# Performance work log

Measured on AMD Instinct MI355X. Metric: run time of the kernel, lower is better.

The kernel has to match this reference:

```python
import jax, jax.numpy as jnp
import numpy as np
import math

LENGTH = 2048
N_LEVEL = int(math.log2(LENGTH))   # 11 butterfly levels
BATCH = 4096
CROSS_T = 1.0      # crossing_transmission_factor (ideal)
CROSS_PHI = 0.0    # crossing_phase_shift (ideal)


def _bitrev(n):
    perm = np.arange(n).reshape(n, 1)
    for _ in range(int(math.log2(n))):
        h = perm.shape[0] // 2
        perm = np.hstack((perm[:h], perm[h:]))
    return perm.squeeze(0)


def _forward_indices(length):
    # ButterflyPermutation.gen_permutation_indices (forward direction)
    nlev = int(math.log2(length)) - 1
    init = np.arange(length)
    idxs = []
    for level in range(nlev):
        bs = 2 ** (level + 2)
        idx = init.reshape(-1, length // bs, 2, bs // 2).transpose(0, 1, 3, 2).reshape(-1)
        idxs.append(idx)
    return idxs


def _crossings(idxs, length):
    # cascaded waveguide-crossing transfer function per level: [length, 2] complex
    out = []
    for idx in idxs:
        n = np.abs(idx - np.arange(length)).astype(np.float32)
        mag = CROSS_T ** n
        phi = n * CROSS_PHI
        out.append(np.stack([mag * np.cos(phi), mag * np.sin(phi)], -1).astype(np.float32))
    return out


BITREV = _bitrev(LENGTH)
FWD_IDX = _forward_indices(LENGTH)
CROSSINGS = [jnp.asarray(c) for c in _crossings(FWD_IDX, LENGTH)]


def complex_mult(a, b):
    ar, ai = a[..., 0], a[..., 1]
    br, bi = b[..., 0], b[..., 1]
    return jnp.stack([ar * br - ai * bi, ar * bi + ai * br], axis=-1)


def setup_inputs() -> dict:
    key = jax.random.key(0)
    kx, kp = jax.random.split(key)
    x = jax.random.normal(kx, (BATCH, LENGTH, 2), dtype=jnp.float32)
    phases = jax.random.normal(kp, (N_LEVEL + 1, LENGTH // 2, 2), dtype=jnp.float32)
    return {"x": x, "phases": phases}


def reference(x, phases):
    # mode='full' coupler transfer function (build_coupler_transfer_function_2)
    ph = phases[:N_LEVEL]                      # [n_level, L/2, 2]
    c1, c2 = jnp.cos(ph[..., 0]), jnp.cos(ph[..., 1])
    s1, s2 = jnp.sin(ph[..., 0]), jnp.sin(ph[..., 1])
    w_real = jnp.stack([c1, -s2, -s1, c2], -1).reshape(N_LEVEL, LENGTH // 2, 2, 2)
    w_imag = jnp.stack([s1, c2, c1, s2], -1).reshape(N_LEVEL, LENGTH // 2, 2, 2)

    out = x[:, BITREV, :]                      # bit-reversal permutation
    for level in range(N_LEVEL):
        v = out.reshape(BATCH, LENGTH // 2, 2, 2)   # [b, pair, j, complex]
        vr, vi = v[..., 0], v[..., 1]
        wr, wi = w_real[level], w_imag[level]
        # complex 2x2 matvec per pair
        r = jnp.einsum('pij,bpj->bpi', wr, vr) - jnp.einsum('pij,bpj->bpi', wi, vi)
        i = jnp.einsum('pij,bpj->bpi', wr, vi) + jnp.einsum('pij,bpj->bpi', wi, vr)
        out = jnp.stack([r, i], -1).reshape(BATCH, LENGTH, 2)
        if level < N_LEVEL - 1:
            # butterfly permutation + crossing transfer (identity when ideal)
            out = complex_mult(CROSSINGS[level][None], out[:, FWD_IDX[level], :])

    # last-level phase shifter: one phase per waveguide
    lp = phases[-1].reshape(LENGTH)
    ps = jnp.stack([jnp.cos(lp), jnp.sin(lp)], -1)  # [L, 2]
    return complex_mult(ps[None], out)
```

## Files before the change

### kernel.cpp

```cpp
#include <hip/hip_runtime.h>


__device__ __forceinline__ unsigned revw(unsigned x, int w) {
    return w ? (__brev(x) >> (32 - w)) : 0u;
}
__device__ __forceinline__ unsigned pmap(unsigned slot, int level) {
    int shift = 10 - level;
    return (revw(slot & ((1u << shift) - 1u), shift) << level) | (slot >> (shift + 1));
}

__global__ void twiddle_kernel(const float* __restrict__ phases, float4* __restrict__ tw) {
    int id = blockIdx.x * 256 + threadIdx.x;
    if (id >= 12288) return;
    float t1, t2;
    if (id < 2048) {
        int t = id & 255, r = id >> 8;
        int b = r & 1, pj = (r >> 1) & 1, lvl = r >> 2;
        unsigned unit = (unsigned)t + ((lvl == 0) ? 256u : 512u) * (unsigned)pj;
        unsigned slot = 2u * unit + (unsigned)b;
        unsigned p = pmap(slot, lvl);
        t1 = phases[(lvl * 1024 + p) * 2 + 0];
        t2 = phases[(lvl * 1024 + p) * 2 + 1];
    } else if (id < 8192) {
        int j2 = id - 2048;
        int sg = j2 / 3072, rem = j2 % 3072;
        int m = rem >> 8, t = rem & 255;
        int L = 2 + 3 * sg;
        int lg = sg ? 3 : 6;
        unsigned H = 1u << lg;
        unsigned s = (((unsigned)t >> lg) << (lg + 3)) | ((unsigned)t & (H - 1));
        int lo = m >> 2, pj = m & 3;
        int j = (lo == 0) ? pj : ((lo == 1) ? ((pj & 1) | ((pj >> 1) << 2)) : (pj << 1));
        unsigned slot = s + (unsigned)j * H;
        int level = L + lo;
        unsigned p = pmap(slot, level);
        t1 = phases[(level * 1024 + p) * 2 + 0];
        t2 = phases[(level * 1024 + p) * 2 + 1];
    } else if (id < 9216) {
        unsigned u = (unsigned)(id - 8192);
        unsigned c0 = 2u * u, c1 = 2u * u + 1u;
        t1 = phases[(8 * 1024 + pmap(c0 & ~4u, 8)) * 2 + ((c0 >> 2) & 1)];
        t2 = phases[(8 * 1024 + pmap(c1 & ~4u, 8)) * 2 + ((c1 >> 2) & 1)];
    } else if (id < 10240) {
        unsigned u = (unsigned)(id - 9216);
        unsigned c0 = 2u * u, c1 = 2u * u + 1u;
        t1 = phases[(9 * 1024 + pmap(c0 & ~2u, 9)) * 2 + ((c0 >> 1) & 1)];
        t2 = phases[(9 * 1024 + pmap(c1 & ~2u, 9)) * 2 + ((c1 >> 1) & 1)];
    } else if (id < 11264) {
        unsigned u = (unsigned)(id - 10240);
        unsigned p = pmap(2u * u, 10);
        t1 = phases[(10 * 1024 + p) * 2 + 0];
        t2 = phases[(10 * 1024 + p) * 2 + 1];
    } else {
        int q = id - 11264;
        t1 = phases[11 * 2048 + q * 2 + 0];
        t2 = phases[11 * 2048 + q * 2 + 1];
    }
    tw[id] = make_float4(cosf(t1), sinf(t1), cosf(t2), sinf(t2));
}

__device__ __forceinline__ void bf(float2 v0, float2 v1, float4 w, float2& o0, float2& o1) {
    float ar = fmaf(w.x, v0.x, -w.y * v0.y);
    float ai = fmaf(w.x, v0.y,  w.y * v0.x);
    float br = fmaf(w.z, v1.x, -w.w * v1.y);
    float bi = fmaf(w.z, v1.y,  w.w * v1.x);
    o0 = make_float2(ar - bi, ai + br);
    o1 = make_float2(br - ai, bi + ar);
}
__device__ __forceinline__ float2 cm(float wc, float ws, float2 z) {
    return make_float2(fmaf(wc, z.x, -ws * z.y), fmaf(wc, z.y, ws * z.x));
}
__device__ __forceinline__ float2 comb(float2 local, float2 recv) {
    return make_float2(local.x - recv.y, local.y + recv.x);
}
__device__ __forceinline__ float2 sx(float2 v, int mask) {
    return make_float2(__shfl_xor(v.x, mask, 64), __shfl_xor(v.y, mask, 64));
}

__device__ __forceinline__ void lvlA(float2 e[8], const float4 w[4]) {
    bf(e[0], e[4], w[0], e[0], e[4]);
    bf(e[1], e[5], w[1], e[1], e[5]);
    bf(e[2], e[6], w[2], e[2], e[6]);
    bf(e[3], e[7], w[3], e[3], e[7]);
}
__device__ __forceinline__ void lvlB(float2 e[8], const float4 w[4]) {
    bf(e[0], e[2], w[0], e[0], e[2]);
    bf(e[1], e[3], w[1], e[1], e[3]);
    bf(e[4], e[6], w[2], e[4], e[6]);
    bf(e[5], e[7], w[3], e[5], e[7]);
}
__device__ __forceinline__ void lvlC(float2 e[8], const float4 w[4]) {
    bf(e[0], e[1], w[0], e[0], e[1]);
    bf(e[2], e[3], w[1], e[2], e[3]);
    bf(e[4], e[5], w[2], e[4], e[5]);
    bf(e[6], e[7], w[3], e[6], e[7]);
}

__device__ __forceinline__ void lbar() {
    asm volatile("s_waitcnt lgkmcnt(0)" ::: "memory");
    __builtin_amdgcn_s_barrier();
}

__global__ __launch_bounds__(256, 4) void bfly_kernel(const float4* __restrict__ x,
                                                      const float4* __restrict__ tw,
                                                      float4* __restrict__ out) {
    __shared__ float4 lds[2048];
    float2* lf = (float2*)lds;
    const unsigned t = threadIdx.x;
    const int rowbase = blockIdx.x * 2048;

    float2 z0[8], z1[8];
    float4 w[4], wn[4];

    {
        const float4* x0 = x + rowbase;
        const float4* x1 = x + rowbase + 1024;
#pragma unroll
        for (int k = 0; k < 4; ++k) {
            float4 u = x0[t + 256u * k];
            z0[2 * k] = make_float2(u.x, u.y); z0[2 * k + 1] = make_float2(u.z, u.w);
        }
#pragma unroll
        for (int k = 0; k < 4; ++k) {
            float4 u = x1[t + 256u * k];
            z1[2 * k] = make_float2(u.x, u.y); z1[2 * k + 1] = make_float2(u.z, u.w);
        }
#pragma unroll
        for (int k = 0; k < 4; ++k) w[k] = tw[k * 256 + t];
        lvlA(z0, w); lvlA(z1, w);
#pragma unroll
        for (int k = 0; k < 4; ++k) w[k] = tw[(4 + k) * 256 + t];
        lvlB(z0, w); lvlB(z1, w);
#pragma unroll
        for (int m = 0; m < 4; ++m) wn[m] = tw[2048 + m * 256 + t];
#pragma unroll
        for (int k = 0; k < 4; ++k) {
            lds[t + 256u * k]        = make_float4(z0[2 * k].x, z0[2 * k].y, z0[2 * k + 1].x, z0[2 * k + 1].y);
            lds[1024 + t + 256u * k] = make_float4(z1[2 * k].x, z1[2 * k].y, z1[2 * k + 1].x, z1[2 * k + 1].y);
        }
    }
    lbar();

    {
        const unsigned s = ((t >> 6) << 9) | (t & 63u);
        float4 wb[4], wc[4];
#pragma unroll
        for (int m = 0; m < 4; ++m) wb[m] = tw[2048 + (4 + m) * 256 + t];
#pragma unroll
        for (int m = 0; m < 4; ++m) wc[m] = tw[2048 + (8 + m) * 256 + t];
#pragma unroll
        for (int j = 0; j < 8; ++j) z0[j] = lf[s + 64u * j];
#pragma unroll
        for (int j = 0; j < 8; ++j) z1[j] = lf[2048 + s + 64u * j];
        lvlA(z0, wn); lvlA(z1, wn);
        lvlB(z0, wb); lvlB(z1, wb);
        lvlC(z0, wc); lvlC(z1, wc);
#pragma unroll
        for (int m = 0; m < 4; ++m) wn[m] = tw[5120 + m * 256 + t];
#pragma unroll
        for (int j = 0; j < 8; ++j) lf[s + 64u * j] = z0[j];
#pragma unroll
        for (int j = 0; j < 8; ++j) lf[2048 + s + 64u * j] = z1[j];
    }
    lbar();

    {
        const unsigned s2 = ((t >> 3) << 6) | (t & 7u);
        float4 wb[4], wc[4];
#pragma unroll
        for (int m = 0; m < 4; ++m) wb[m] = tw[5120 + (4 + m) * 256 + t];
#pragma unroll
        for (int m = 0; m < 4; ++m) wc[m] = tw[5120 + (8 + m) * 256 + t];
#pragma unroll
        for (int j = 0; j < 8; ++j) z0[j] = lf[s2 + 8u * j];
#pragma unroll
        for (int j = 0; j < 8; ++j) z1[j] = lf[2048 + s2 + 8u * j];
        lvlA(z0, wn); lvlA(z1, wn);
        lvlB(z0, wb); lvlB(z1, wb);
        lvlC(z0, wc); lvlC(z1, wc);
#pragma unroll
        for (int g = 0; g < 4; ++g) wn[g] = tw[8192 + t + 256u * g];
#pragma unroll
        for (int j = 0; j < 8; ++j) lf[s2 + 8u * j] = z0[j];
#pragma unroll
        for (int j = 0; j < 8; ++j) lf[2048 + s2 + 8u * j] = z1[j];
    }
    lbar();

#pragma unroll
    for (int g = 0; g < 4; ++g) {
        const unsigned u = t + 256u * g;
        float4 w9 = tw[9216 + u];
        float4 wA = tw[10240 + u];
        float4 p  = tw[11264 + u];
        float4 q0 = lds[u];
        float4 q1 = lds[1024 + u];
        float2 x00 = make_float2(q0.x, q0.y), x01 = make_float2(q0.z, q0.w);
        float2 x10 = make_float2(q1.x, q1.y), x11 = make_float2(q1.z, q1.w);
        float4 w8 = wn[g];
        float2 a00 = cm(w8.x, w8.y, x00), a01 = cm(w8.z, w8.w, x01);
        float2 a10 = cm(w8.x, w8.y, x10), a11 = cm(w8.z, w8.w, x11);
        x00 = comb(a00, sx(a00, 2)); x01 = comb(a01, sx(a01, 2));
        x10 = comb(a10, sx(a10, 2)); x11 = comb(a11, sx(a11, 2));
        a00 = cm(w9.x, w9.y, x00); a01 = cm(w9.z, w9.w, x01);
        a10 = cm(w9.x, w9.y, x10); a11 = cm(w9.z, w9.w, x11);
        x00 = comb(a00, sx(a00, 1)); x01 = comb(a01, sx(a01, 1));
        x10 = comb(a10, sx(a10, 1)); x11 = comb(a11, sx(a11, 1));
        bf(x00, x01, wA, x00, x01);
        bf(x10, x11, wA, x10, x11);
        out[rowbase + u] = make_float4(
            fmaf(p.x, x00.x, -p.y * x00.y), fmaf(p.x, x00.y, p.y * x00.x),
            fmaf(p.z, x01.x, -p.w * x01.y), fmaf(p.z, x01.y, p.w * x01.x));
        out[rowbase + 1024 + u] = make_float4(
            fmaf(p.x, x10.x, -p.y * x10.y), fmaf(p.x, x10.y, p.y * x10.x),
            fmaf(p.z, x11.x, -p.w * x11.y), fmaf(p.z, x11.y, p.w * x11.x));
    }
}

extern "C" void kernel_launch(void* const* d_in, const int* in_sizes, int n_in,
                              void* d_out, int out_size, void* d_ws, size_t ws_size,
                              hipStream_t stream) {
    const float* x = (const float*)d_in[0];
    const float* phases = (const float*)d_in[1];
    float4* tw = (float4*)d_ws;

    twiddle_kernel<<<48, 256, 0, stream>>>(phases, tw);
    bfly_kernel<<<2048, 256, 0, stream>>>((const float4*)x, tw, (float4*)d_out);
}
```

Measured before the change: 42.41 us.

## Interleave paired rows in LDS as float4 with XOR swizzle

Shared memory is relaid so each float4 slot holds the same complex element from both rows a block processes. The middle stages then issue one 128-bit LDS access per element instead of two 64-bit ones, and an XOR swizzle on the slot index is meant to spread the strided accesses across banks. Launch bounds are also raised from 4 to 5 waves per SIMD. The higher occupancy target tightens the register budget and could cause spills.

```diff
diff --git a/kernel.cpp b/kernel.cpp
--- a/kernel.cpp
+++ b/kernel.cpp
@@ -96,16 +96,17 @@
     bf(e[6], e[7], w[3], e[6], e[7]);
 }
 
+__device__ __forceinline__ unsigned swz(unsigned U) { return U ^ ((U >> 3) & 7u); }
+
 __device__ __forceinline__ void lbar() {
     asm volatile("s_waitcnt lgkmcnt(0)" ::: "memory");
     __builtin_amdgcn_s_barrier();
 }
 
-__global__ __launch_bounds__(256, 4) void bfly_kernel(const float4* __restrict__ x,
+__global__ __launch_bounds__(256, 5) void bfly_kernel(const float4* __restrict__ x,
                                                       const float4* __restrict__ tw,
                                                       float4* __restrict__ out) {
-    __shared__ float4 lds[2048];
-    float2* lf = (float2*)lds;
+    __shared__ float4 lds4[2048];
     const unsigned t = threadIdx.x;
     const int rowbase = blockIdx.x * 2048;
 
@@ -135,8 +136,9 @@
         for (int m = 0; m < 4; ++m) wn[m] = tw[2048 + m * 256 + t];
 #pragma unroll
         for (int k = 0; k < 4; ++k) {
-            lds[t + 256u * k]        = make_float4(z0[2 * k].x, z0[2 * k].y, z0[2 * k + 1].x, z0[2 * k + 1].y);
-            lds[1024 + t + 256u * k] = make_float4(z1[2 * k].x, z1[2 * k].y, z1[2 * k + 1].x, z1[2 * k + 1].y);
+            unsigned c = 2u * (t + 256u * k);
+            lds4[swz(c)]     = make_float4(z0[2 * k].x, z0[2 * k].y, z1[2 * k].x, z1[2 * k].y);
+            lds4[swz(c + 1)] = make_float4(z0[2 * k + 1].x, z0[2 * k + 1].y, z1[2 * k + 1].x, z1[2 * k + 1].y);
         }
     }
     lbar();
@@ -149,18 +151,18 @@
 #pragma unroll
         for (int m = 0; m < 4; ++m) wc[m] = tw[2048 + (8 + m) * 256 + t];
 #pragma unroll
-        for (int j = 0; j < 8; ++j) z0[j] = lf[s + 64u * j];
-#pragma unroll
-        for (int j = 0; j < 8; ++j) z1[j] = lf[2048 + s + 64u * j];
+        for (int j = 0; j < 8; ++j) {
+            float4 q = lds4[swz(s + 64u * j)];
+            z0[j] = make_float2(q.x, q.y); z1[j] = make_float2(q.z, q.w);
+        }
         lvlA(z0, wn); lvlA(z1, wn);
         lvlB(z0, wb); lvlB(z1, wb);
         lvlC(z0, wc); lvlC(z1, wc);
 #pragma unroll
         for (int m = 0; m < 4; ++m) wn[m] = tw[5120 + m * 256 + t];
 #pragma unroll
-        for (int j = 0; j < 8; ++j) lf[s + 64u * j] = z0[j];
-#pragma unroll
-        for (int j = 0; j < 8; ++j) lf[2048 + s + 64u * j] = z1[j];
+        for (int j = 0; j < 8; ++j)
+            lds4[swz(s + 64u * j)] = make_float4(z0[j].x, z0[j].y, z1[j].x, z1[j].y);
     }
     lbar();
 
@@ -172,32 +174,32 @@
 #pragma unroll
         for (int m = 0; m < 4; ++m) wc[m] = tw[5120 + (8 + m) * 256 + t];
 #pragma unroll
-        for (int j = 0; j < 8; ++j) z0[j] = lf[s2 + 8u * j];
-#pragma unroll
-        for (int j = 0; j < 8; ++j) z1[j] = lf[2048 + s2 + 8u * j];
+        for (int j = 0; j < 8; ++j) {
+            float4 q = lds4[swz(s2 + 8u * j)];
+            z0[j] = make_float2(q.x, q.y); z1[j] = make_float2(q.z, q.w);
+        }
         lvlA(z0, wn); lvlA(z1, wn);
         lvlB(z0, wb); lvlB(z1, wb);
         lvlC(z0, wc); lvlC(z1, wc);
 #pragma unroll
         for (int g = 0; g < 4; ++g) wn[g] = tw[8192 + t + 256u * g];
 #pragma unroll
-        for (int j = 0; j < 8; ++j) lf[s2 + 8u * j] = z0[j];
-#pragma unroll
-        for (int j = 0; j < 8; ++j) lf[2048 + s2 + 8u * j] = z1[j];
+        for (int j = 0; j < 8; ++j)
+            lds4[swz(s2 + 8u * j)] = make_float4(z0[j].x, z0[j].y, z1[j].x, z1[j].y);
     }
     lbar();
 
 #pragma unroll
     for (int g = 0; g < 4; ++g) {
         const unsigned u = t + 256u * g;
+        float4 w8 = wn[g];
         float4 w9 = tw[9216 + u];
         float4 wA = tw[10240 + u];
         float4 p  = tw[11264 + u];
-        float4 q0 = lds[u];
-        float4 q1 = lds[1024 + u];
-        float2 x00 = make_float2(q0.x, q0.y), x01 = make_float2(q0.z, q0.w);
-        float2 x10 = make_float2(q1.x, q1.y), x11 = make_float2(q1.z, q1.w);
-        float4 w8 = wn[g];
+        float4 q0 = lds4[swz(2u * u)];
+        float4 q1 = lds4[swz(2u * u + 1)];
+        float2 x00 = make_float2(q0.x, q0.y), x01 = make_float2(q1.x, q1.y);
+        float2 x10 = make_float2(q0.z, q0.w), x11 = make_float2(q1.z, q1.w);
         float2 a00 = cm(w8.x, w8.y, x00), a01 = cm(w8.z, w8.w, x01);
         float2 a10 = cm(w8.x, w8.y, x10), a11 = cm(w8.z, w8.w, x11);
         x00 = comb(a00, sx(a00, 2)); x01 = comb(a01, sx(a01, 2));
```

Measured after the change: 42.49 us. No clear change (+0.2%).
